# Performance work log

Hardware: AMD Instinct MI355X
Metric: run time of the kernel (lower is better)

The kernel has to match this reference:

```python
import jax, jax.numpy as jnp
import numpy as np

B, L, C, H, OUT = 256, 65, 32, 128, 32   # batch, spline knots, input ch, hidden ch, output ch
STEP = 1.0                               # rk4 fixed step size; interval is [0, L-1]


def setup_inputs() -> dict:
    key = jax.random.key(0)
    ks = jax.random.split(key, 8)

    def w(k, shape, fan_in):
        return jax.random.normal(k, shape, jnp.float32) / np.float32(np.sqrt(fan_in))

    return dict(
        coeffs=jax.random.normal(ks[0], (B, L - 1, 4 * C), jnp.float32),
        x_last=jax.random.normal(ks[1], (B, OUT), jnp.float32),
        Wi=w(ks[2], (C, H), C), bi=jnp.zeros((H,), jnp.float32),
        W1=w(ks[3], (H, H), H), b1=jnp.zeros((H,), jnp.float32),
        W2=w(ks[4], (H, H), H), b2=jnp.zeros((H,), jnp.float32),
        W3=w(ks[5], (H, H * C), H), b3=jnp.zeros((H * C,), jnp.float32),
        Wr=w(ks[6], (H, OUT), H), br=jnp.zeros((OUT,), jnp.float32),
    )


def reference(coeffs, x_last, Wi, bi, W1, b1, W2, b2, W3, b3, Wr, br):
    Bn, Lm1, _ = coeffs.shape
    # torchcde CubicSpline coefficient layout: [a, b, two_c, three_d]
    a, bb, two_c, three_d = jnp.split(coeffs, 4, axis=-1)  # each (B, L-1, C)

    def deriv(t):  # dX/dt at scalar time t -> (B, C)
        idx = jnp.clip(jnp.floor(t), 0.0, Lm1 - 1.0).astype(jnp.int32)
        frac = t - idx
        return bb[:, idx, :] + (two_c[:, idx, :] + three_d[:, idx, :] * frac) * frac

    def func(z):  # CDEFunc: 3-layer MLP -> (B, H, C)
        h = jax.nn.softplus(z @ W1 + b1)
        h = jax.nn.softplus(h @ W2 + b2)
        return jnp.tanh(h @ W3 + b3).reshape(Bn, H, C)

    def vf(t, z):  # f(t, z) @ dX/dt  -> (B, H)
        return jnp.einsum('bhc,bc->bh', func(z), deriv(t))

    # z0 = initial(X(t0)); X(0) lies on piece 0 with frac 0 -> a[:, 0]
    z0 = a[:, 0, :] @ Wi + bi

    # torchdiffeq fixed grid: t0, t0+h, ..., t1  (step_size=1 -> L points)
    ts = jnp.asarray(np.arange(L, dtype=np.float32) * STEP)
    tpairs = jnp.stack([ts[:-1], ts[1:]], axis=1)  # (L-1, 2)

    def step(z, tp):  # torchdiffeq 'rk4' uses the 3/8-rule (rk4_alt_step_func)
        t0, t1 = tp[0], tp[1]
        dt = t1 - t0
        k1 = vf(t0, z)
        k2 = vf(t0 + dt / 3, z + dt * k1 / 3)
        k3 = vf(t0 + 2 * dt / 3, z + dt * (k2 - k1 / 3))
        k4 = vf(t1, z + dt * (k1 - k2 + k3))
        return z + (k1 + 3.0 * (k2 + k3) + k4) * (dt * 0.125), None

    zT, _ = jax.lax.scan(step, z0, tpairs)
    return x_last + (zT @ Wr + br)
```

## Files before the change

kernel.cpp:

```cpp
#include <hip/hip_runtime.h>
#include <math.h>

typedef __attribute__((ext_vector_type(8))) short v8s;
typedef __attribute__((ext_vector_type(4))) short v4s;
typedef __attribute__((ext_vector_type(4))) float v4f;

#define AP 136
#define OFF_W3 0
#define OFF_WI 524288
#define OFF_W1 528384
#define OFF_W2 544768
#define OFF_WR 561152
#define LO     565248
#define WF_TOTAL2 1130496
#define KBUF_BYTE 2260992
#define FLG_BYTE  2523136
#define WS_END    2527232
#define PREP_W    565248
#define PREP_Z    33280
#define PREP_TOT  598528

static __device__ __forceinline__ float bf2f(unsigned short s){
    union { unsigned u; float f; } v; v.u = ((unsigned)s) << 16; return v.f;
}
static __device__ __forceinline__ unsigned short f2bf(float f){
    union { float ff; unsigned u; } v; v.ff = f;
    return (unsigned short)((v.u + 0x7FFFu + ((v.u >> 16) & 1u)) >> 16);
}
static __device__ __forceinline__ void split3(float v, unsigned short& h,
                                              unsigned short& m, unsigned short& l){
    h = f2bf(v);  float r1 = v - bf2f(h);
    m = f2bf(r1); float r2 = r1 - bf2f(m);
    l = f2bf(r2);
}
static __device__ __forceinline__ float softplus_f(float x){
    float t = __builtin_amdgcn_exp2f(x * 1.44269504088896341f);
    float r = 0.69314718055994531f * __builtin_amdgcn_logf(1.0f + t);
    return (x > 20.0f) ? x : r;
}
static __device__ __forceinline__ float tanh_f(float x){
    float xc = fminf(fmaxf(x, -9.0f), 9.0f);
    float t = __builtin_amdgcn_exp2f(xc * 2.8853900817779268f);
    float d = t + 1.0f;
    float r = __builtin_amdgcn_rcpf(d);
    r = r * (2.0f - d * r);
    return (t - 1.0f) * r;
}

#define MFMA(acc, a, b) acc = __builtin_amdgcn_mfma_f32_16x16x32_bf16(a, b, acc, 0, 0, 0)

__global__ void prep_kernel(const float* __restrict__ W3,
                            const float* __restrict__ Wi,
                            const float* __restrict__ W1,
                            const float* __restrict__ W2,
                            const float* __restrict__ Wr,
                            unsigned short* __restrict__ dst,
                            int wlimit, unsigned long long wsbytes){
    int g = blockIdx.x * 256 + threadIdx.x;
    if (g >= PREP_TOT) return;
    if (g >= PREP_W){
        int t = g - PREP_W;
        unsigned long long byte = (unsigned long long)KBUF_BYTE + (unsigned long long)t * 8ull;
        if (t < PREP_Z && byte + 8ull <= wsbytes)
            *(unsigned long long*)((char*)dst + byte) = 0ull;
        return;
    }

    const float* W; int KT, N, t;
    if      (g < OFF_WI){ W = W3; KT = 4; N = 4096; t = g; }
    else if (g < OFF_W1){ W = Wi; KT = 1; N = 128;  t = g - OFF_WI; }
    else if (g < OFF_W2){ W = W1; KT = 4; N = 128;  t = g - OFF_W1; }
    else if (g < OFF_WR){ W = W2; KT = 4; N = 128;  t = g - OFF_W2; }
    else               { W = Wr; KT = 4; N = 32;   t = g - OFF_WR; }

    int j  = t & 7;
    int l  = (t >> 3) & 63;
    int t2 = t >> 9;
    int kt = t2 % KT;
    int nt = t2 / KT;
    int row = kt * 32 + (l >> 4) * 8 + j;
    int col = nt * 16 + (l & 15);
    float w = W[(size_t)row * N + col];
    unsigned short h = f2bf(w);
    if (g < wlimit)      dst[g]      = h;
    if (g + LO < wlimit) dst[g + LO] = f2bf(w - bf2f(h));
}

template<int KT, int MODE>
static __device__ __forceinline__ void gemm1(
    const unsigned short* __restrict__ wf, int wbase, int ntiles,
    const unsigned short* Ah, const unsigned short* Am, const unsigned short* Al,
    unsigned short* Aoh, unsigned short* Aom, unsigned short* Aol,
    float* zx,
    const float* __restrict__ bias_g,
    const float* __restrict__ xlast, float* __restrict__ outg, int bg)
{
    const int tid  = threadIdx.x;
    const int lane = tid & 63;
    const int wid  = tid >> 6;
    const int l15  = lane & 15;
    const int q    = lane >> 4;
    if (wid >= ntiles) return;
    const int nt = wid;

    v8s ah[KT], am[KT], al[KT];
#pragma unroll
    for (int kt = 0; kt < KT; ++kt){
        ah[kt] = *(const v8s*)&Ah[l15 * AP + kt * 32 + q * 8];
        am[kt] = *(const v8s*)&Am[l15 * AP + kt * 32 + q * 8];
        al[kt] = *(const v8s*)&Al[l15 * AP + kt * 32 + q * 8];
    }

    v4f acc = {0.f, 0.f, 0.f, 0.f};
#pragma unroll
    for (int kt = 0; kt < KT; ++kt){
        int o = wbase + ((nt * KT + kt) * 64 + lane) * 8;
        v8s bh = *(const v8s*)&wf[o];
        v8s bl = *(const v8s*)&wf[o + LO];
        MFMA(acc, ah[kt], bh); MFMA(acc, am[kt], bh); MFMA(acc, al[kt], bh);
        MFMA(acc, ah[kt], bl); MFMA(acc, am[kt], bl);
    }
    const int c0 = nt * 16 + l15;

    if (MODE == 0){
#pragma unroll
        for (int r = 0; r < 4; ++r){
            int b = q * 4 + r;
            zx[b * 128 + c0] = acc[r] + bias_g[c0];
        }
    } else if (MODE == 1){
#pragma unroll
        for (int r = 0; r < 4; ++r){
            int b = q * 4 + r;
            float v0 = softplus_f(acc[r] + bias_g[c0]);
            unsigned short h, m, l;
            split3(v0, h, m, l);
            Aoh[b*AP+c0] = h; Aom[b*AP+c0] = m; Aol[b*AP+c0] = l;
        }
    } else {
#pragma unroll
        for (int r = 0; r < 4; ++r){
            int b = q * 4 + r, gb = bg * 16 + b;
            outg[gb * 32 + c0] = acc[r] + bias_g[c0] + xlast[gb * 32 + c0];
        }
    }
}

__global__ __launch_bounds__(512, 1) void cde_kernel(
    const float* __restrict__ coeffs,
    const float* __restrict__ x_last,
    const float* __restrict__ bi,
    const float* __restrict__ b1,
    const float* __restrict__ b2,
    const float* __restrict__ b3,
    const float* __restrict__ br,
    const unsigned short* __restrict__ wf,
    float* __restrict__ kbuf,
    unsigned int* __restrict__ flgs,
    float* __restrict__ outg)
{
    __shared__ unsigned short A0h[16*AP] __attribute__((aligned(16)));
    __shared__ unsigned short A0m[16*AP] __attribute__((aligned(16)));
    __shared__ unsigned short A0l[16*AP] __attribute__((aligned(16)));
    __shared__ unsigned short A1h[16*AP] __attribute__((aligned(16)));
    __shared__ unsigned short A1m[16*AP] __attribute__((aligned(16)));
    __shared__ unsigned short A1l[16*AP] __attribute__((aligned(16)));
    __shared__ unsigned short A2h[16*AP] __attribute__((aligned(16)));
    __shared__ unsigned short A2m[16*AP] __attribute__((aligned(16)));
    __shared__ unsigned short A2l[16*AP] __attribute__((aligned(16)));
    __shared__ float dval[512];
    __shared__ float zx[2048];

    const int tid  = threadIdx.x;
    const int lane = tid & 63;
    const int wid  = tid >> 6;
    const int l15  = lane & 15;
    const int q    = lane >> 4;
    const int bx   = blockIdx.x;
    const int bg   = (bx & 7) * 2 + (bx >> 7);
    const int tr   = (bx >> 3) & 15;

    float*        kb0     = kbuf + bg * 4096;
    unsigned int* teamflg = flgs + bg * 64;
    unsigned int* myflag  = teamflg + tr * 4;

    for (int e = tid; e < 16*AP; e += 512){
        A0h[e]=0; A0m[e]=0; A0l[e]=0; A1h[e]=0; A1m[e]=0; A1l[e]=0;
        A2h[e]=0; A2m[e]=0; A2l[e]=0;
    }

    v8s w3h[2][4], w3l[2][4];
    float b3v[2];
    {
        const int p = wid;
#pragma unroll
        for (int i = 0; i < 2; ++i){
            int ntg = tr * 16 + 2 * p + i;
#pragma unroll
            for (int kt = 0; kt < 4; ++kt){
                int o = ((ntg * 4 + kt) * 64 + lane) * 8;
                w3h[i][kt] = *(const v8s*)&wf[o];
                w3l[i][kt] = *(const v8s*)&wf[o + LO];
            }
        }
        int cg0 = tr * 256 + p * 32 + l15;
        b3v[0] = b3[cg0]; b3v[1] = b3[cg0 + 16];
    }

    const int arow = tid >> 5;
    const int acol = (tid & 31) * 4;
    const int e0r  = tid >> 5, e0c = tid & 31;

    {
        float v = coeffs[((size_t)(bg * 16 + e0r) * 64) * 128 + e0c];
        unsigned short h, m, l; split3(v, h, m, l);
        A0h[e0r*AP+e0c] = h; A0m[e0r*AP+e0c] = m; A0l[e0r*AP+e0c] = l;
    }
    __syncthreads();
    gemm1<1, 0>(wf, OFF_WI, 8, A0h, A0m, A0l, nullptr, nullptr, nullptr,
                zx, bi, nullptr, nullptr, bg);
    __syncthreads();

    float zp[4], kap[4], k1p[4], k2p[4];
#pragma unroll
    for (int i = 0; i < 4; ++i){ zp[i] = zx[tid*4 + i]; kap[i]=0.f; k1p[i]=0.f; k2p[i]=0.f; }

    {
        size_t base = ((size_t)(bg * 16 + e0r) * 64 + 0) * 128;
        dval[tid] = coeffs[base + 32 + e0c];
        v4s vh, vm, vl;
#pragma unroll
        for (int i = 0; i < 4; ++i){
            unsigned short h, m, l; split3(zp[i], h, m, l);
            vh[i] = (short)h; vm[i] = (short)m; vl[i] = (short)l;
        }
        *(v4s*)&A0h[arow*AP + acol] = vh;
        *(v4s*)&A0m[arow*AP + acol] = vm;
        *(v4s*)&A0l[arow*AP + acol] = vl;
    }

    for (int st = 0; st < 256; ++st){
        const int sub = st & 3;
        __syncthreads();
        gemm1<4, 1>(wf, OFF_W1, 8, A0h, A0m, A0l, A1h, A1m, A1l,
                    nullptr, b1, nullptr, nullptr, bg);
        __syncthreads();
        gemm1<4, 1>(wf, OFF_W2, 8, A1h, A1m, A1l, A2h, A2m, A2l,
                    nullptr, b2, nullptr, nullptr, bg);
        __syncthreads();
        float* kbw = kb0 + (st & 1) * 2048;
        {
            v8s ah[4], am[4], al[4];
#pragma unroll
            for (int kt = 0; kt < 4; ++kt){
                ah[kt] = *(const v8s*)&A2h[l15*AP + kt*32 + q*8];
                am[kt] = *(const v8s*)&A2m[l15*AP + kt*32 + q*8];
                al[kt] = *(const v8s*)&A2l[l15*AP + kt*32 + q*8];
            }
            v4f acc0 = {0.f,0.f,0.f,0.f}, acc1 = {0.f,0.f,0.f,0.f};
#pragma unroll
            for (int kt = 0; kt < 4; ++kt){
                MFMA(acc0, ah[kt], w3h[0][kt]); MFMA(acc0, am[kt], w3h[0][kt]);
                MFMA(acc0, al[kt], w3h[0][kt]);
                MFMA(acc0, ah[kt], w3l[0][kt]); MFMA(acc0, am[kt], w3l[0][kt]);
                MFMA(acc1, ah[kt], w3h[1][kt]); MFMA(acc1, am[kt], w3h[1][kt]);
                MFMA(acc1, al[kt], w3h[1][kt]);
                MFMA(acc1, ah[kt], w3l[1][kt]); MFMA(acc1, am[kt], w3l[1][kt]);
            }
            float s4[4];
#pragma unroll
            for (int r = 0; r < 4; ++r){
                float u0 = acc0[r] + b3v[0];
                float u1 = acc1[r] + b3v[1];
                s4[r] = tanh_f(u0) * dval[(q*4 + r) * 32 + l15]
                      + tanh_f(u1) * dval[(q*4 + r) * 32 + 16 + l15];
            }
#pragma unroll
            for (int sm = 1; sm <= 8; sm <<= 1){
#pragma unroll
                for (int r = 0; r < 4; ++r) s4[r] += __shfl_xor(s4[r], sm);
            }
            if (l15 == 0){
#pragma unroll
                for (int r = 0; r < 4; ++r)
                    __hip_atomic_store(&kbw[(q*4 + r) * 128 + tr * 8 + wid], s4[r],
                                       __ATOMIC_RELAXED, __HIP_MEMORY_SCOPE_AGENT);
            }
            asm volatile("s_waitcnt vmcnt(0)" ::: "memory");
            __syncthreads();
            if (tid == 0)
                __hip_atomic_store(myflag, (unsigned)(st + 1),
                                   __ATOMIC_RELAXED, __HIP_MEMORY_SCOPE_AGENT);
        }

        const int stp1 = (st < 255) ? st + 1 : 255;
        const int sp   = stp1 >> 2, sb = stp1 & 3;
        int nidx; float nfrac;
        if      (sb == 0){ nidx = sp; nfrac = 0.f; }
        else if (sb == 1){ nidx = sp; nfrac = 1.f / 3.f; }
        else if (sb == 2){ nidx = sp; nfrac = 2.f / 3.f; }
        else { nidx = (sp < 63) ? sp + 1 : 63; nfrac = (sp < 63) ? 0.f : 1.f; }
        float cb0, cc0, cd0;
        {
            size_t base = ((size_t)(bg * 16 + e0r) * 64 + nidx) * 128;
            cb0 = coeffs[base + 32 + e0c];
            cc0 = coeffs[base + 64 + e0c];
            cd0 = coeffs[base + 96 + e0c];
        }

        {
            const unsigned tgt = (unsigned)(st + 1);
            const unsigned int* fp = &teamflg[((tid & 31) >> 1) * 4];
            unsigned it = 0;
            while (__hip_atomic_load(fp, __ATOMIC_RELAXED,
                                     __HIP_MEMORY_SCOPE_AGENT) < tgt
                   && ++it < (1u << 22))
                __builtin_amdgcn_s_sleep(1);
        }

        float kv[4];
#pragma unroll
        for (int i = 0; i < 2; ++i){
            union { unsigned long long u; float f[2]; } pk;
            pk.u = __hip_atomic_load((const unsigned long long*)&kbw[tid*4 + 2*i],
                                     __ATOMIC_RELAXED, __HIP_MEMORY_SCOPE_AGENT);
            kv[2*i] = pk.f[0]; kv[2*i+1] = pk.f[1];
        }
#pragma unroll
        for (int i = 0; i < 4; ++i){
            float k = kv[i];
            if      (sub == 0){ k1p[i] = k; kap[i] = zp[i] + k * (1.f/3.f); }
            else if (sub == 1){ k2p[i] = k; kap[i] = zp[i] + (k - k1p[i] * (1.f/3.f)); }
            else if (sub == 2){ kap[i] = zp[i] + (k1p[i] - k2p[i] + k); }
            else { zp[i] = zp[i] + (6.f*k2p[i] - 2.f*k1p[i]
                                    + 3.f*(kap[i] - zp[i]) + k) * 0.125f; }
        }

        dval[tid] = cb0 + (cc0 + cd0 * nfrac) * nfrac;
        {
            const int nsub = stp1 & 3;
            v4s vh, vm, vl;
#pragma unroll
            for (int i = 0; i < 4; ++i){
                float v = (nsub == 0) ? zp[i] : kap[i];
                unsigned short h, m, l; split3(v, h, m, l);
                vh[i] = (short)h; vm[i] = (short)m; vl[i] = (short)l;
            }
            *(v4s*)&A0h[arow*AP + acol] = vh;
            *(v4s*)&A0m[arow*AP + acol] = vm;
            *(v4s*)&A0l[arow*AP + acol] = vl;
        }
    }

    {
        v4s vh, vm, vl;
#pragma unroll
        for (int i = 0; i < 4; ++i){
            unsigned short h, m, l; split3(zp[i], h, m, l);
            vh[i] = (short)h; vm[i] = (short)m; vl[i] = (short)l;
        }
        *(v4s*)&A0h[arow*AP + acol] = vh;
        *(v4s*)&A0m[arow*AP + acol] = vm;
        *(v4s*)&A0l[arow*AP + acol] = vl;
    }
    __syncthreads();
    gemm1<4, 4>(wf, OFF_WR, 2, A0h, A0m, A0l, nullptr, nullptr, nullptr,
                nullptr, br, x_last, outg, bg);
}

extern "C" void kernel_launch(void* const* d_in, const int* in_sizes, int n_in,
                              void* d_out, int out_size, void* d_ws, size_t ws_size,
                              hipStream_t stream)
{
    const float* coeffs = (const float*)d_in[0];
    const float* x_last = (const float*)d_in[1];
    const float* Wi     = (const float*)d_in[2];
    const float* bi     = (const float*)d_in[3];
    const float* W1     = (const float*)d_in[4];
    const float* b1     = (const float*)d_in[5];
    const float* W2     = (const float*)d_in[6];
    const float* b2     = (const float*)d_in[7];
    const float* W3     = (const float*)d_in[8];
    const float* b3     = (const float*)d_in[9];
    const float* Wr     = (const float*)d_in[10];
    const float* br     = (const float*)d_in[11];
    unsigned short* wf   = (unsigned short*)d_ws;
    float*          kbuf = (float*)((char*)d_ws + KBUF_BYTE);
    unsigned int*   flgs = (unsigned int*)((char*)d_ws + FLG_BYTE);

    size_t wcap = ws_size / 2;
    int wl = (wcap > (size_t)WF_TOTAL2) ? WF_TOTAL2 : (int)wcap;

    prep_kernel<<<(PREP_TOT + 255) / 256, 256, 0, stream>>>(W3, Wi, W1, W2, Wr,
                                                            wf, wl,
                                                            (unsigned long long)ws_size);
    cde_kernel<<<256, 512, 0, stream>>>(coeffs, x_last, bi, b1, b2, b3, br, wf,
                                        kbuf, flgs, (float*)d_out);
}
```

Measured before the change: 1.389 ms.

## Double block size to 1024 threads, splitting each MFMA tile's epilogue rows across wave pairs

Each block now runs 16 waves instead of 8. Each pair of waves computes the same 16x16 MFMA tile redundantly, and each wave handles only 2 of the 4 accumulator rows in the epilogue (softplus/tanh, split3, stores). The per-thread state update and the shared A-matrix writes are halved, using 2-element vectors. The aim is to shorten the serial epilogue and state-update work on the per-step critical path. In exchange the MFMA work and weight loads are duplicated, there are more waves at each barrier, and register pressure rises with the looser launch bounds.

```diff
diff --git a/kernel.cpp b/kernel.cpp
--- a/kernel.cpp
+++ b/kernel.cpp
@@ -2,7 +2,7 @@
 #include <math.h>
 
 typedef __attribute__((ext_vector_type(8))) short v8s;
-typedef __attribute__((ext_vector_type(4))) short v4s;
+typedef __attribute__((ext_vector_type(2))) short v2s;
 typedef __attribute__((ext_vector_type(4))) float v4f;
 
 #define AP 136
@@ -100,8 +100,9 @@
     const int wid  = tid >> 6;
     const int l15  = lane & 15;
     const int q    = lane >> 4;
-    if (wid >= ntiles) return;
-    const int nt = wid;
+    const int nt   = wid & 7;
+    const int rlo  = (wid >> 3) * 2;
+    if (nt >= ntiles) return;
 
     v8s ah[KT], am[KT], al[KT];
 #pragma unroll
@@ -124,14 +125,14 @@
 
     if (MODE == 0){
 #pragma unroll
-        for (int r = 0; r < 4; ++r){
-            int b = q * 4 + r;
+        for (int rr = 0; rr < 2; ++rr){
+            int r = rlo + rr, b = q * 4 + r;
             zx[b * 128 + c0] = acc[r] + bias_g[c0];
         }
     } else if (MODE == 1){
 #pragma unroll
-        for (int r = 0; r < 4; ++r){
-            int b = q * 4 + r;
+        for (int rr = 0; rr < 2; ++rr){
+            int r = rlo + rr, b = q * 4 + r;
             float v0 = softplus_f(acc[r] + bias_g[c0]);
             unsigned short h, m, l;
             split3(v0, h, m, l);
@@ -139,14 +140,14 @@
         }
     } else {
 #pragma unroll
-        for (int r = 0; r < 4; ++r){
-            int b = q * 4 + r, gb = bg * 16 + b;
+        for (int rr = 0; rr < 2; ++rr){
+            int r = rlo + rr, b = q * 4 + r, gb = bg * 16 + b;
             outg[gb * 32 + c0] = acc[r] + bias_g[c0] + xlast[gb * 32 + c0];
         }
     }
 }
 
-__global__ __launch_bounds__(512, 1) void cde_kernel(
+__global__ __launch_bounds__(1024) void cde_kernel(
     const float* __restrict__ coeffs,
     const float* __restrict__ x_last,
     const float* __restrict__ bi,
@@ -176,6 +177,8 @@
     const int wid  = tid >> 6;
     const int l15  = lane & 15;
     const int q    = lane >> 4;
+    const int wid8 = wid & 7;
+    const int rlo  = (wid >> 3) * 2;
     const int bx   = blockIdx.x;
     const int bg   = (bx & 7) * 2 + (bx >> 7);
     const int tr   = (bx >> 3) & 15;
@@ -184,7 +187,7 @@
     unsigned int* teamflg = flgs + bg * 64;
     unsigned int* myflag  = teamflg + tr * 4;
 
-    for (int e = tid; e < 16*AP; e += 512){
+    for (int e = tid; e < 16*AP; e += 1024){
         A0h[e]=0; A0m[e]=0; A0l[e]=0; A1h[e]=0; A1m[e]=0; A1l[e]=0;
         A2h[e]=0; A2m[e]=0; A2l[e]=0;
     }
@@ -192,7 +195,7 @@
     v8s w3h[2][4], w3l[2][4];
     float b3v[2];
     {
-        const int p = wid;
+        const int p = wid8;
 #pragma unroll
         for (int i = 0; i < 2; ++i){
             int ntg = tr * 16 + 2 * p + i;
@@ -207,11 +210,11 @@
         b3v[0] = b3[cg0]; b3v[1] = b3[cg0 + 16];
     }
 
-    const int arow = tid >> 5;
-    const int acol = (tid & 31) * 4;
-    const int e0r  = tid >> 5, e0c = tid & 31;
-
-    {
+    const int arow = tid >> 6;
+    const int acol = (tid & 63) * 2;
+    const int e0r  = (tid >> 5) & 15, e0c = tid & 31;
+
+    if (tid < 512){
         float v = coeffs[((size_t)(bg * 16 + e0r) * 64) * 128 + e0c];
         unsigned short h, m, l; split3(v, h, m, l);
         A0h[e0r*AP+e0c] = h; A0m[e0r*AP+e0c] = m; A0l[e0r*AP+e0c] = l;
@@ -221,22 +224,24 @@
                 zx, bi, nullptr, nullptr, bg);
     __syncthreads();
 
-    float zp[4], kap[4], k1p[4], k2p[4];
-#pragma unroll
-    for (int i = 0; i < 4; ++i){ zp[i] = zx[tid*4 + i]; kap[i]=0.f; k1p[i]=0.f; k2p[i]=0.f; }
+    float zp[2], kap[2], k1p[2], k2p[2];
+#pragma unroll
+    for (int i = 0; i < 2; ++i){ zp[i] = zx[tid*2 + i]; kap[i]=0.f; k1p[i]=0.f; k2p[i]=0.f; }
 
     {
-        size_t base = ((size_t)(bg * 16 + e0r) * 64 + 0) * 128;
-        dval[tid] = coeffs[base + 32 + e0c];
-        v4s vh, vm, vl;
-#pragma unroll
-        for (int i = 0; i < 4; ++i){
+        if (tid < 512){
+            size_t base = ((size_t)(bg * 16 + e0r) * 64 + 0) * 128;
+            dval[tid] = coeffs[base + 32 + e0c];
+        }
+        v2s vh, vm, vl;
+#pragma unroll
+        for (int i = 0; i < 2; ++i){
             unsigned short h, m, l; split3(zp[i], h, m, l);
             vh[i] = (short)h; vm[i] = (short)m; vl[i] = (short)l;
         }
-        *(v4s*)&A0h[arow*AP + acol] = vh;
-        *(v4s*)&A0m[arow*AP + acol] = vm;
-        *(v4s*)&A0l[arow*AP + acol] = vl;
+        *(v2s*)&A0h[arow*AP + acol] = vh;
+        *(v2s*)&A0m[arow*AP + acol] = vm;
+        *(v2s*)&A0l[arow*AP + acol] = vl;
     }
 
     for (int st = 0; st < 256; ++st){
@@ -267,24 +272,27 @@
                 MFMA(acc1, al[kt], w3h[1][kt]);
                 MFMA(acc1, ah[kt], w3l[1][kt]); MFMA(acc1, am[kt], w3l[1][kt]);
             }
-            float s4[4];
-#pragma unroll
-            for (int r = 0; r < 4; ++r){
+            float s4[2];
+#pragma unroll
+            for (int rr = 0; rr < 2; ++rr){
+                int r = rlo + rr;
                 float u0 = acc0[r] + b3v[0];
                 float u1 = acc1[r] + b3v[1];
-                s4[r] = tanh_f(u0) * dval[(q*4 + r) * 32 + l15]
-                      + tanh_f(u1) * dval[(q*4 + r) * 32 + 16 + l15];
+                s4[rr] = tanh_f(u0) * dval[(q*4 + r) * 32 + l15]
+                       + tanh_f(u1) * dval[(q*4 + r) * 32 + 16 + l15];
             }
 #pragma unroll
             for (int sm = 1; sm <= 8; sm <<= 1){
 #pragma unroll
-                for (int r = 0; r < 4; ++r) s4[r] += __shfl_xor(s4[r], sm);
+                for (int rr = 0; rr < 2; ++rr) s4[rr] += __shfl_xor(s4[rr], sm);
             }
             if (l15 == 0){
 #pragma unroll
-                for (int r = 0; r < 4; ++r)
-                    __hip_atomic_store(&kbw[(q*4 + r) * 128 + tr * 8 + wid], s4[r],
+                for (int rr = 0; rr < 2; ++rr){
+                    int r = rlo + rr;
+                    __hip_atomic_store(&kbw[(q*4 + r) * 128 + tr * 8 + wid8], s4[rr],
                                        __ATOMIC_RELAXED, __HIP_MEMORY_SCOPE_AGENT);
+                }
             }
             asm volatile("s_waitcnt vmcnt(0)" ::: "memory");
             __syncthreads();
@@ -300,8 +308,8 @@
         else if (sb == 1){ nidx = sp; nfrac = 1.f / 3.f; }
         else if (sb == 2){ nidx = sp; nfrac = 2.f / 3.f; }
         else { nidx = (sp < 63) ? sp + 1 : 63; nfrac = (sp < 63) ? 0.f : 1.f; }
-        float cb0, cc0, cd0;
-        {
+        float cb0 = 0.f, cc0 = 0.f, cd0 = 0.f;
+        if (tid < 512){
             size_t base = ((size_t)(bg * 16 + e0r) * 64 + nidx) * 128;
             cb0 = coeffs[base + 32 + e0c];
             cc0 = coeffs[base + 64 + e0c];
@@ -310,7 +318,7 @@
 
         {
             const unsigned tgt = (unsigned)(st + 1);
-            const unsigned int* fp = &teamflg[((tid & 31) >> 1) * 4];
+            const unsigned int* fp = &teamflg[((tid & 63) >> 2) * 4];
             unsigned it = 0;
             while (__hip_atomic_load(fp, __ATOMIC_RELAXED,
                                      __HIP_MEMORY_SCOPE_AGENT) < tgt
@@ -318,16 +326,15 @@
                 __builtin_amdgcn_s_sleep(1);
         }
 
-        float kv[4];
+        float kv[2];
+        {
+            union { unsigned long long u; float f[2]; } pk;
+            pk.u = __hip_atomic_load((const unsigned long long*)&kbw[tid*2],
+                                     __ATOMIC_RELAXED, __HIP_MEMORY_SCOPE_AGENT);
+            kv[0] = pk.f[0]; kv[1] = pk.f[1];
+        }
 #pragma unroll
         for (int i = 0; i < 2; ++i){
-            union { unsigned long long u; float f[2]; } pk;
-            pk.u = __hip_atomic_load((const unsigned long long*)&kbw[tid*4 + 2*i],
-                                     __ATOMIC_RELAXED, __HIP_MEMORY_SCOPE_AGENT);
-            kv[2*i] = pk.f[0]; kv[2*i+1] = pk.f[1];
-        }
-#pragma unroll
-        for (int i = 0; i < 4; ++i){
             float k = kv[i];
             if      (sub == 0){ k1p[i] = k; kap[i] = zp[i] + k * (1.f/3.f); }
             else if (sub == 1){ k2p[i] = k; kap[i] = zp[i] + (k - k1p[i] * (1.f/3.f)); }
@@ -336,32 +343,33 @@
                                     + 3.f*(kap[i] - zp[i]) + k) * 0.125f; }
         }
 
-        dval[tid] = cb0 + (cc0 + cd0 * nfrac) * nfrac;
+        if (tid < 512)
+            dval[tid] = cb0 + (cc0 + cd0 * nfrac) * nfrac;
         {
             const int nsub = stp1 & 3;
-            v4s vh, vm, vl;
-#pragma unroll
-            for (int i = 0; i < 4; ++i){
+            v2s vh, vm, vl;
+#pragma unroll
+            for (int i = 0; i < 2; ++i){
                 float v = (nsub == 0) ? zp[i] : kap[i];
                 unsigned short h, m, l; split3(v, h, m, l);
                 vh[i] = (short)h; vm[i] = (short)m; vl[i] = (short)l;
             }
-            *(v4s*)&A0h[arow*AP + acol] = vh;
-            *(v4s*)&A0m[arow*AP + acol] = vm;
-            *(v4s*)&A0l[arow*AP + acol] = vl;
+            *(v2s*)&A0h[arow*AP + acol] = vh;
+            *(v2s*)&A0m[arow*AP + acol] = vm;
+            *(v2s*)&A0l[arow*AP + acol] = vl;
         }
     }
 
     {
-        v4s vh, vm, vl;
-#pragma unroll
-        for (int i = 0; i < 4; ++i){
+        v2s vh, vm, vl;
+#pragma unroll
+        for (int i = 0; i < 2; ++i){
             unsigned short h, m, l; split3(zp[i], h, m, l);
             vh[i] = (short)h; vm[i] = (short)m; vl[i] = (short)l;
         }
-        *(v4s*)&A0h[arow*AP + acol] = vh;
-        *(v4s*)&A0m[arow*AP + acol] = vm;
-        *(v4s*)&A0l[arow*AP + acol] = vl;
+        *(v2s*)&A0h[arow*AP + acol] = vh;
+        *(v2s*)&A0m[arow*AP + acol] = vm;
+        *(v2s*)&A0l[arow*AP + acol] = vl;
     }
     __syncthreads();
     gemm1<4, 4>(wf, OFF_WR, 2, A0h, A0m, A0l, nullptr, nullptr, nullptr,
@@ -394,6 +402,6 @@
     prep_kernel<<<(PREP_TOT + 255) / 256, 256, 0, stream>>>(W3, Wi, W1, W2, Wr,
                                                             wf, wl,
                                                             (unsigned long long)ws_size);
-    cde_kernel<<<256, 512, 0, stream>>>(coeffs, x_last, bi, b1, b2, b3, br, wf,
-                                        kbuf, flgs, (float*)d_out);
-}
+    cde_kernel<<<256, 1024, 0, stream>>>(coeffs, x_last, bi, b1, b2, b3, br, wf,
+                                         kbuf, flgs, (float*)d_out);
+}
```

New measurement: 5.250 ms. 3.78x slower.
